# Kernel tuning notes

Hardware: AMD Instinct MI355X
Metric: run time of the kernel (lower is better)

Reference implementation:

```python
import jax, jax.numpy as jnp
import numpy as np

B, D, U = 8192, 1024, 1024


def setup_inputs() -> dict:
    key = jax.random.key(0)
    ks = jax.random.split(key, 11)
    scale = 0.05  # keras 'random_normal' initializer default stddev
    inp = {
        "inputs": jax.random.normal(ks[0], (B, D), jnp.float32),
        "h_tm1": jax.random.normal(ks[1], (B, U), jnp.float32),
        "c_tm1": jax.random.normal(ks[2], (B, U), jnp.float32),
        "W_i": jax.random.normal(ks[3], (D, U), jnp.float32) * scale,
        "U_i": jax.random.normal(ks[4], (U, U), jnp.float32) * scale,
        "b_i": jnp.zeros((U,), jnp.float32),
        "W_f": jax.random.normal(ks[5], (D, U), jnp.float32) * scale,
        "U_f": jax.random.normal(ks[6], (U, U), jnp.float32) * scale,
        "b_f": jnp.zeros((U,), jnp.float32),
        "W_c": jax.random.normal(ks[7], (D, U), jnp.float32) * scale,
        "U_c": jax.random.normal(ks[8], (U, U), jnp.float32) * scale,
        "b_c": jnp.zeros((U,), jnp.float32),
        "W_o": jax.random.normal(ks[9], (D, U), jnp.float32) * scale,
        "U_o": jax.random.normal(ks[10], (U, U), jnp.float32) * scale,
        "b_o": jnp.zeros((U,), jnp.float32),
    }
    return inp


def reference(inputs, h_tm1, c_tm1, W_i, U_i, b_i, W_f, U_f, b_f, W_c, U_c, b_c, W_o, U_o, b_o):
    # Concatenate the 4 gate projections into single GEMMs (same math, fused form)
    Wx = jnp.concatenate([W_i, W_f, W_c, W_o], axis=1)  # [D, 4U]
    Uh = jnp.concatenate([U_i, U_f, U_c, U_o], axis=1)  # [U, 4U]
    b = jnp.concatenate([b_i, b_f, b_c, b_o], axis=0)   # [4U]
    z = inputs @ Wx + h_tm1 @ Uh + b                     # [B, 4U]
    u = W_i.shape[1]
    zi, zf, zc, zo = z[:, :u], z[:, u:2 * u], z[:, 2 * u:3 * u], z[:, 3 * u:]
    i = jax.nn.sigmoid(zi)
    f = jax.nn.sigmoid(zf)
    c_ = jnp.tanh(zc)
    c = f * c_tm1 + i * c_
    o = jax.nn.sigmoid(zo)
    h = o * jnp.tanh(c)
    return (h, c)
```

## Files before the change

### kernel.cpp

```cpp
#include <hip/hip_runtime.h>
#include <hip/hip_bf16.h>
#include <cstdint>


using f32x4  = __attribute__((ext_vector_type(4))) float;
using short8 = __attribute__((ext_vector_type(8))) short;

__device__ __forceinline__ unsigned short f2bf(float f) {
  union { float f; unsigned int u; } v; v.f = f;
  unsigned int r = v.u + 0x7fffu + ((v.u >> 16) & 1u);
  return (unsigned short)(r >> 16);
}
__device__ __forceinline__ float sigmoidf_fast(float x) { return 1.f / (1.f + __expf(-x)); }
__device__ __forceinline__ float tanhf_fast(float x)    { return 1.f - 2.f / (__expf(2.f * x) + 1.f); }

__global__ void conv_a_kernel(const float* __restrict__ X, const float* __restrict__ H,
                              unsigned short* __restrict__ Abf) {
  int idx = blockIdx.x * blockDim.x + threadIdx.x;
  int b  = idx >> 8;
  int kq = (idx & 255) << 2;
  float4 x = *(const float4*)(X + (long)b * 1024 + kq);
  float4 h = *(const float4*)(H + (long)b * 1024 + kq);
  ushort4 xo, ho;
  xo.x = f2bf(x.x); xo.y = f2bf(x.y); xo.z = f2bf(x.z); xo.w = f2bf(x.w);
  ho.x = f2bf(h.x); ho.y = f2bf(h.y); ho.z = f2bf(h.z); ho.w = f2bf(h.w);
  *(ushort4*)(Abf + (long)b * 2048 + kq)        = xo;
  *(ushort4*)(Abf + (long)b * 2048 + 1024 + kq) = ho;
}

__global__ void conv_b_kernel(const float* W_i, const float* U_i,
                              const float* W_f, const float* U_f,
                              const float* W_c, const float* U_c,
                              const float* W_o, const float* U_o,
                              unsigned short* __restrict__ Bt) {
  __shared__ float tile[64][65];
  int z = blockIdx.z;
  const float* src;
  switch (z) {
    case 0: src = W_i; break; case 1: src = U_i; break;
    case 2: src = W_f; break; case 3: src = U_f; break;
    case 4: src = W_c; break; case 5: src = U_c; break;
    case 6: src = W_o; break; default: src = U_o; break;
  }
  int g = z >> 1, s = z & 1;
  int k0 = blockIdx.x * 64;
  int u0 = blockIdx.y * 64;
  int t = threadIdx.x;
  int c = t & 63, r0 = t >> 6;
#pragma unroll
  for (int i = 0; i < 16; ++i) {
    int r = i * 4 + r0;
    tile[r][c] = src[(long)(k0 + r) * 1024 + u0 + c];
  }
  __syncthreads();
  int ul = t >> 2;
  int ks = (t & 3) * 16;
  unsigned short outv[16];
#pragma unroll
  for (int j = 0; j < 16; ++j) outv[j] = f2bf(tile[ks + j][ul]);
  long n   = 4L * u0 + (ul >> 4) * 64 + g * 16 + (ul & 15);
  long col = (long)s * 1024 + k0 + ks;
  uint4* dst = (uint4*)(Bt + n * 2048 + col);
  dst[0] = *(uint4*)(outv);
  dst[1] = *(uint4*)(outv + 8);
}

__global__ __launch_bounds__(512) void lstm_gemm_kernel(
    const unsigned short* __restrict__ Abf,
    const unsigned short* __restrict__ Btbf,
    const float* __restrict__ b_i, const float* __restrict__ b_f,
    const float* __restrict__ b_c, const float* __restrict__ b_o,
    const float* __restrict__ c_tm1,
    float* __restrict__ outH, float* __restrict__ outC) {
  __shared__ unsigned short smem[3 * 16384];

  int bid = blockIdx.x;
  int swz = (bid & 7) * 64 + (bid >> 3);
  int bm = swz >> 4;
  int bn = swz & 15;

  int t = threadIdx.x;
  int lane = t & 63;
  int w = t >> 6;
  int wm = w >> 2;
  int wn = w & 3;
  int rl = lane & 15;
  int kg = lane >> 4;

#define AOFF(MI) ((wm * 128 + (MI) * 16 + rl) * 32 + \
    ((((kg * 16) ^ ((((wm * 128 + (MI) * 16 + rl) >> 1) & 3) << 4))) >> 1))
#define BOFF(NI) ((wn * 64 + (NI) * 16 + rl) * 32 + \
    ((((kg * 16) ^ ((((wn * 64 + (NI) * 16 + rl) >> 1) & 3) << 4))) >> 1))
  const int offA0 = AOFF(0), offA1 = AOFF(1), offA2 = AOFF(2), offA3 = AOFF(3);
  const int offA4 = AOFF(4), offA5 = AOFF(5), offA6 = AOFF(6), offA7 = AOFF(7);
  const int offB0 = 8192 + BOFF(0), offB1 = 8192 + BOFF(1);
  const int offB2 = 8192 + BOFF(2), offB3 = 8192 + BOFF(3);
#undef AOFF
#undef BOFF

  int srow = t >> 2;
  int cbe  = (((t & 3) * 16) ^ (((srow >> 1) & 3) << 4)) >> 1;
  const unsigned short* aS0 = Abf  + (long)(bm * 256 + srow) * 2048 + cbe;
  const unsigned short* aS1 = aS0 + 128L * 2048;
  const unsigned short* bS0 = Btbf + (long)(bn * 256 + srow) * 2048 + cbe;
  const unsigned short* bS1 = bS0 + 128L * 2048;
  const int dstA0 = t * 8, dstA1 = 4096 + t * 8;
  const int dstB0 = 8192 + t * 8, dstB1 = 12288 + t * 8;

#define GLL(SRC, SB, DOFF)                                                                     \
  __builtin_amdgcn_global_load_lds((const __attribute__((address_space(1))) void*)(SRC),       \
      (__attribute__((address_space(3))) void*)(&smem[(SB) * 16384 + (DOFF)]), 16, 0, 0)

  f32x4 acc[8][4];
#pragma unroll
  for (int mi = 0; mi < 8; ++mi)
#pragma unroll
    for (int ni = 0; ni < 4; ++ni) acc[mi][ni] = (f32x4){0.f, 0.f, 0.f, 0.f};

  GLL(aS0, 0, dstA0); GLL(aS1, 0, dstA1); GLL(bS0, 0, dstB0); GLL(bS1, 0, dstB1);
  GLL(aS0 + 32, 1, dstA0); GLL(aS1 + 32, 1, dstA1);
  GLL(bS0 + 32, 1, dstB0); GLL(bS1 + 32, 1, dstB1);
  asm volatile("s_waitcnt vmcnt(4)" ::: "memory");
  __builtin_amdgcn_s_barrier();
  aS0 += 64; aS1 += 64; bS0 += 64; bS1 += 64;

#define MF_ROW(AF, MI)                                                                  \
  acc[MI][0] = __builtin_amdgcn_mfma_f32_16x16x32_bf16(AF, bfr0, acc[MI][0], 0, 0, 0);  \
  acc[MI][1] = __builtin_amdgcn_mfma_f32_16x16x32_bf16(AF, bfr1, acc[MI][1], 0, 0, 0);  \
  acc[MI][2] = __builtin_amdgcn_mfma_f32_16x16x32_bf16(AF, bfr2, acc[MI][2], 0, 0, 0);  \
  acc[MI][3] = __builtin_amdgcn_mfma_f32_16x16x32_bf16(AF, bfr3, acc[MI][3], 0, 0, 0);

#define ITER(RBUF, SBUF, KOFF, DOSTAGE, VMN)                                   \
  do {                                                                         \
    const unsigned short* As_ = smem + (RBUF) * 16384;                         \
                      \
    short8 bfr0 = *(const short8*)(As_ + offB0);                               \
    short8 bfr1 = *(const short8*)(As_ + offB1);                               \
    short8 bfr2 = *(const short8*)(As_ + offB2);                               \
    short8 bfr3 = *(const short8*)(As_ + offB3);                               \
    short8 a0_ = *(const short8*)(As_ + offA0);                                \
    short8 a1_ = *(const short8*)(As_ + offA1);                                \
    short8 a2_ = *(const short8*)(As_ + offA2);                                \
    short8 a3_ = *(const short8*)(As_ + offA3);                                \
    if (DOSTAGE) { GLL(aS0 + (KOFF), (SBUF), dstA0); GLL(aS1 + (KOFF), (SBUF), dstA1); } \
    __builtin_amdgcn_s_barrier();                                              \
    asm volatile("s_waitcnt lgkmcnt(0)" ::: "memory");                         \
    __builtin_amdgcn_sched_barrier(0);                                         \
    __builtin_amdgcn_s_setprio(1);                                             \
    MF_ROW(a0_, 0) MF_ROW(a1_, 1) MF_ROW(a2_, 2) MF_ROW(a3_, 3)                \
    __builtin_amdgcn_s_setprio(0);                                             \
    __builtin_amdgcn_sched_barrier(0);                                         \
    __builtin_amdgcn_s_barrier();                                              \
                 \
    short8 a4_ = *(const short8*)(As_ + offA4);                                \
    short8 a5_ = *(const short8*)(As_ + offA5);                                \
    short8 a6_ = *(const short8*)(As_ + offA6);                                \
    short8 a7_ = *(const short8*)(As_ + offA7);                                \
    if (DOSTAGE) { GLL(bS0 + (KOFF), (SBUF), dstB0); GLL(bS1 + (KOFF), (SBUF), dstB1); } \
    if ((VMN) == 4) asm volatile("s_waitcnt vmcnt(4)" ::: "memory");           \
    if ((VMN) == 0) asm volatile("s_waitcnt vmcnt(0)" ::: "memory");           \
    __builtin_amdgcn_s_barrier();                                              \
    asm volatile("s_waitcnt lgkmcnt(0)" ::: "memory");                         \
    __builtin_amdgcn_sched_barrier(0);                                         \
    __builtin_amdgcn_s_setprio(1);                                             \
    MF_ROW(a4_, 4) MF_ROW(a5_, 5) MF_ROW(a6_, 6) MF_ROW(a7_, 7)                \
    __builtin_amdgcn_s_setprio(0);                                             \
    __builtin_amdgcn_sched_barrier(0);                                         \
    __builtin_amdgcn_s_barrier();                                              \
  } while (0)

  for (int g = 0; g < 20; ++g) {
    ITER(0, 2, 0,  1, 4);
    ITER(1, 0, 32, 1, 4);
    ITER(2, 1, 64, 1, 4);
    aS0 += 96; aS1 += 96; bS0 += 96; bS1 += 96;
  }
  ITER(0, 2, 0,  1, 4);
  ITER(1, 0, 32, 1, 4);
  ITER(2, 0, 0,  0, 0);
  ITER(0, 0, 0,  0, -1);
#undef ITER
#undef MF_ROW
#undef GLL

  int mbase = bm * 256 + wm * 128;
  int nbase = bn * 256 + wn * 64;
  int u = (nbase >> 2) + rl;
  float bi_v = b_i[u], bf_v = b_f[u], bc_v = b_c[u], bo_v = b_o[u];
  int rquad = (lane >> 4) << 2;
#pragma unroll
  for (int mi = 0; mi < 8; ++mi) {
#pragma unroll
    for (int j = 0; j < 4; ++j) {
      int brow = mbase + mi * 16 + rquad + j;
      float zi = acc[mi][0][j] + bi_v;
      float zf = acc[mi][1][j] + bf_v;
      float zc = acc[mi][2][j] + bc_v;
      float zo = acc[mi][3][j] + bo_v;
      float ig = sigmoidf_fast(zi);
      float fg = sigmoidf_fast(zf);
      float cg = tanhf_fast(zc);
      float og = sigmoidf_fast(zo);
      float cp = c_tm1[(long)brow * 1024 + u];
      float cn = fg * cp + ig * cg;
      float hn = og * tanhf_fast(cn);
      outH[(long)brow * 1024 + u] = hn;
      outC[(long)brow * 1024 + u] = cn;
    }
  }
}

extern "C" void kernel_launch(void* const* d_in, const int* in_sizes, int n_in,
                              void* d_out, int out_size, void* d_ws, size_t ws_size,
                              hipStream_t stream) {
  (void)in_sizes; (void)n_in; (void)out_size; (void)ws_size;
  const float* X   = (const float*)d_in[0];
  const float* Hst = (const float*)d_in[1];
  const float* Cst = (const float*)d_in[2];
  const float* W_i = (const float*)d_in[3];
  const float* U_i = (const float*)d_in[4];
  const float* b_i = (const float*)d_in[5];
  const float* W_f = (const float*)d_in[6];
  const float* U_f = (const float*)d_in[7];
  const float* b_f = (const float*)d_in[8];
  const float* W_c = (const float*)d_in[9];
  const float* U_c = (const float*)d_in[10];
  const float* b_c = (const float*)d_in[11];
  const float* W_o = (const float*)d_in[12];
  const float* U_o = (const float*)d_in[13];
  const float* b_o = (const float*)d_in[14];

  unsigned short* Abf  = (unsigned short*)d_ws;
  unsigned short* Btbf = (unsigned short*)((char*)d_ws + 33554432);

  float* outH = (float*)d_out;
  float* outC = outH + 8192L * 1024;

  conv_a_kernel<<<8192, 256, 0, stream>>>(X, Hst, Abf);
  conv_b_kernel<<<dim3(16, 16, 8), 256, 0, stream>>>(W_i, U_i, W_f, U_f, W_c, U_c, W_o, U_o, Btbf);
  lstm_gemm_kernel<<<512, 512, 0, stream>>>(Abf, Btbf, b_i, b_f, b_c, b_o, Cst, outH, outC);
}
```

Measured before the change: 164.4 us.

## Register-prefetch next LDS fragments and halve barriers in LSTM GEMM main loop

Restructures the GEMM k-loop so the A/B fragments for the next stage are loaded from LDS into a second register set (ping-pong p/q) while the current stage's MFMAs run. It cuts the barriers per k-step from four to one, issues all four global-to-LDS loads together after a vmcnt(0) wait, and unrolls the loop by six stages. It also sets launch_bounds(512,2), which caps registers to allow two blocks per CU. The extra fragment registers under a tighter register cap risk spills. The vmcnt(0) wait each step may also expose global load latency.

```diff
diff --git a/kernel.cpp b/kernel.cpp
--- a/kernel.cpp
+++ b/kernel.cpp
@@ -65,7 +65,7 @@
   dst[1] = *(uint4*)(outv + 8);
 }
 
-__global__ __launch_bounds__(512) void lstm_gemm_kernel(
+__global__ __launch_bounds__(512, 2) void lstm_gemm_kernel(
     const unsigned short* __restrict__ Abf,
     const unsigned short* __restrict__ Btbf,
     const float* __restrict__ b_i, const float* __restrict__ b_f,
@@ -117,70 +117,86 @@
 #pragma unroll
     for (int ni = 0; ni < 4; ++ni) acc[mi][ni] = (f32x4){0.f, 0.f, 0.f, 0.f};
 
+  short8 pa0, pa1, pa2, pa3, pb0, pb1, pb2, pb3;
+  short8 qa0, qa1, qa2, qa3, qb0, qb1, qb2, qb3;
+  short8 ah0, ah1, ah2, ah3;
+
   GLL(aS0, 0, dstA0); GLL(aS1, 0, dstA1); GLL(bS0, 0, dstB0); GLL(bS1, 0, dstB1);
   GLL(aS0 + 32, 1, dstA0); GLL(aS1 + 32, 1, dstA1);
   GLL(bS0 + 32, 1, dstB0); GLL(bS1 + 32, 1, dstB1);
   asm volatile("s_waitcnt vmcnt(4)" ::: "memory");
   __builtin_amdgcn_s_barrier();
+  pa0 = *(const short8*)(smem + offA0);
+  pa1 = *(const short8*)(smem + offA1);
+  pa2 = *(const short8*)(smem + offA2);
+  pa3 = *(const short8*)(smem + offA3);
+  pb0 = *(const short8*)(smem + offB0);
+  pb1 = *(const short8*)(smem + offB1);
+  pb2 = *(const short8*)(smem + offB2);
+  pb3 = *(const short8*)(smem + offB3);
   aS0 += 64; aS1 += 64; bS0 += 64; bS1 += 64;
 
-#define MF_ROW(AF, MI)                                                                  \
-  acc[MI][0] = __builtin_amdgcn_mfma_f32_16x16x32_bf16(AF, bfr0, acc[MI][0], 0, 0, 0);  \
-  acc[MI][1] = __builtin_amdgcn_mfma_f32_16x16x32_bf16(AF, bfr1, acc[MI][1], 0, 0, 0);  \
-  acc[MI][2] = __builtin_amdgcn_mfma_f32_16x16x32_bf16(AF, bfr2, acc[MI][2], 0, 0, 0);  \
-  acc[MI][3] = __builtin_amdgcn_mfma_f32_16x16x32_bf16(AF, bfr3, acc[MI][3], 0, 0, 0);
-
-#define ITER(RBUF, SBUF, KOFF, DOSTAGE, VMN)                                   \
+#define MF4(AF, MI, BP)                                                                      \
+  acc[MI][0] = __builtin_amdgcn_mfma_f32_16x16x32_bf16(AF, BP##0, acc[MI][0], 0, 0, 0);      \
+  acc[MI][1] = __builtin_amdgcn_mfma_f32_16x16x32_bf16(AF, BP##1, acc[MI][1], 0, 0, 0);      \
+  acc[MI][2] = __builtin_amdgcn_mfma_f32_16x16x32_bf16(AF, BP##2, acc[MI][2], 0, 0, 0);      \
+  acc[MI][3] = __builtin_amdgcn_mfma_f32_16x16x32_bf16(AF, BP##3, acc[MI][3], 0, 0, 0);
+
+#define ITER(BUF, STG, NXT, KOFF, C, N, DOSTAGE, DOPREF, DOSYNC)               \
   do {                                                                         \
-    const unsigned short* As_ = smem + (RBUF) * 16384;                         \
-                      \
-    short8 bfr0 = *(const short8*)(As_ + offB0);                               \
-    short8 bfr1 = *(const short8*)(As_ + offB1);                               \
-    short8 bfr2 = *(const short8*)(As_ + offB2);                               \
-    short8 bfr3 = *(const short8*)(As_ + offB3);                               \
-    short8 a0_ = *(const short8*)(As_ + offA0);                                \
-    short8 a1_ = *(const short8*)(As_ + offA1);                                \
-    short8 a2_ = *(const short8*)(As_ + offA2);                                \
-    short8 a3_ = *(const short8*)(As_ + offA3);                                \
-    if (DOSTAGE) { GLL(aS0 + (KOFF), (SBUF), dstA0); GLL(aS1 + (KOFF), (SBUF), dstA1); } \
-    __builtin_amdgcn_s_barrier();                                              \
-    asm volatile("s_waitcnt lgkmcnt(0)" ::: "memory");                         \
+    const unsigned short* Sr_ = smem + (BUF) * 16384;                          \
+    ah0 = *(const short8*)(Sr_ + offA4);                                       \
+    ah1 = *(const short8*)(Sr_ + offA5);                                       \
+    ah2 = *(const short8*)(Sr_ + offA6);                                       \
+    ah3 = *(const short8*)(Sr_ + offA7);                                       \
     __builtin_amdgcn_sched_barrier(0);                                         \
     __builtin_amdgcn_s_setprio(1);                                             \
-    MF_ROW(a0_, 0) MF_ROW(a1_, 1) MF_ROW(a2_, 2) MF_ROW(a3_, 3)                \
+    MF4(C##a0, 0, C##b) MF4(C##a1, 1, C##b)                                    \
+    MF4(C##a2, 2, C##b) MF4(C##a3, 3, C##b)                                    \
     __builtin_amdgcn_s_setprio(0);                                             \
     __builtin_amdgcn_sched_barrier(0);                                         \
-    __builtin_amdgcn_s_barrier();                                              \
-                 \
-    short8 a4_ = *(const short8*)(As_ + offA4);                                \
-    short8 a5_ = *(const short8*)(As_ + offA5);                                \
-    short8 a6_ = *(const short8*)(As_ + offA6);                                \
-    short8 a7_ = *(const short8*)(As_ + offA7);                                \
-    if (DOSTAGE) { GLL(bS0 + (KOFF), (SBUF), dstB0); GLL(bS1 + (KOFF), (SBUF), dstB1); } \
-    if ((VMN) == 4) asm volatile("s_waitcnt vmcnt(4)" ::: "memory");           \
-    if ((VMN) == 0) asm volatile("s_waitcnt vmcnt(0)" ::: "memory");           \
-    __builtin_amdgcn_s_barrier();                                              \
-    asm volatile("s_waitcnt lgkmcnt(0)" ::: "memory");                         \
+    if (DOSYNC) {                                                              \
+      asm volatile("s_waitcnt vmcnt(0)" ::: "memory");                         \
+      __builtin_amdgcn_s_barrier();                                            \
+      __builtin_amdgcn_sched_barrier(0);                                       \
+    }                                                                          \
+    if (DOSTAGE) {                                                             \
+      GLL(aS0 + (KOFF), (STG), dstA0); GLL(aS1 + (KOFF), (STG), dstA1);        \
+      GLL(bS0 + (KOFF), (STG), dstB0); GLL(bS1 + (KOFF), (STG), dstB1);        \
+    }                                                                          \
+    if (DOPREF) {                                                              \
+      const unsigned short* Sn_ = smem + (NXT) * 16384;                        \
+      N##a0 = *(const short8*)(Sn_ + offA0);                                   \
+      N##a1 = *(const short8*)(Sn_ + offA1);                                   \
+      N##a2 = *(const short8*)(Sn_ + offA2);                                   \
+      N##a3 = *(const short8*)(Sn_ + offA3);                                   \
+      N##b0 = *(const short8*)(Sn_ + offB0);                                   \
+      N##b1 = *(const short8*)(Sn_ + offB1);                                   \
+      N##b2 = *(const short8*)(Sn_ + offB2);                                   \
+      N##b3 = *(const short8*)(Sn_ + offB3);                                   \
+    }                                                                          \
     __builtin_amdgcn_sched_barrier(0);                                         \
     __builtin_amdgcn_s_setprio(1);                                             \
-    MF_ROW(a4_, 4) MF_ROW(a5_, 5) MF_ROW(a6_, 6) MF_ROW(a7_, 7)                \
+    MF4(ah0, 4, C##b) MF4(ah1, 5, C##b)                                        \
+    MF4(ah2, 6, C##b) MF4(ah3, 7, C##b)                                        \
     __builtin_amdgcn_s_setprio(0);                                             \
-    __builtin_amdgcn_sched_barrier(0);                                         \
-    __builtin_amdgcn_s_barrier();                                              \
   } while (0)
 
-  for (int g = 0; g < 20; ++g) {
-    ITER(0, 2, 0,  1, 4);
-    ITER(1, 0, 32, 1, 4);
-    ITER(2, 1, 64, 1, 4);
-    aS0 += 96; aS1 += 96; bS0 += 96; bS1 += 96;
-  }
-  ITER(0, 2, 0,  1, 4);
-  ITER(1, 0, 32, 1, 4);
-  ITER(2, 0, 0,  0, 0);
-  ITER(0, 0, 0,  0, -1);
+  for (int g = 0; g < 10; ++g) {
+    ITER(0, 2, 1, 0,   p, q, 1, 1, 1);
+    ITER(1, 0, 2, 32,  q, p, 1, 1, 1);
+    ITER(2, 1, 0, 64,  p, q, 1, 1, 1);
+    ITER(0, 2, 1, 96,  q, p, 1, 1, 1);
+    ITER(1, 0, 2, 128, p, q, 1, 1, 1);
+    ITER(2, 1, 0, 160, q, p, 1, 1, 1);
+    aS0 += 192; aS1 += 192; bS0 += 192; bS1 += 192;
+  }
+  ITER(0, 2, 1, 0,  p, q, 1, 1, 1);
+  ITER(1, 0, 2, 32, q, p, 1, 1, 1);
+  ITER(2, 0, 0, 0,  p, q, 0, 1, 1);
+  ITER(0, 0, 0, 0,  q, p, 0, 0, 0);
 #undef ITER
-#undef MF_ROW
+#undef MF4
 #undef GLL
 
   int mbase = bm * 256 + wm * 128;
```

Result: no change. 164.7 us (+0.2%).

## Restructure GEMM pipeline to 4-stage K-half LDS buffering with two blocks per CU

Applied to the files above, without the earlier changes.

Replaces the 3-buffer rotating LDS pipeline with a 4-deep pipeline split into separate A and B regions, each stage holding a 32-wide K slice, and rewrites the main loop as explicit phases that issue global-to-LDS loads further ahead. Adds a launch bound of 2 blocks per CU to limit register use. The goal is deeper prefetch to hide global load latency. The trade-off is that LDS grows to 128KB per block, which may prevent two blocks from actually co-residing, and the tighter register cap could cause spills.

```diff
diff --git a/kernel.cpp b/kernel.cpp
--- a/kernel.cpp
+++ b/kernel.cpp
@@ -65,14 +65,14 @@
   dst[1] = *(uint4*)(outv + 8);
 }
 
-__global__ __launch_bounds__(512) void lstm_gemm_kernel(
+__global__ __launch_bounds__(512, 2) void lstm_gemm_kernel(
     const unsigned short* __restrict__ Abf,
     const unsigned short* __restrict__ Btbf,
     const float* __restrict__ b_i, const float* __restrict__ b_f,
     const float* __restrict__ b_c, const float* __restrict__ b_o,
     const float* __restrict__ c_tm1,
     float* __restrict__ outH, float* __restrict__ outC) {
-  __shared__ unsigned short smem[3 * 16384];
+  __shared__ unsigned short smem[65536];
 
   int bid = blockIdx.x;
   int swz = (bid & 7) * 64 + (bid >> 3);
@@ -87,29 +87,39 @@
   int rl = lane & 15;
   int kg = lane >> 4;
 
-#define AOFF(MI) ((wm * 128 + (MI) * 16 + rl) * 32 + \
-    ((((kg * 16) ^ ((((wm * 128 + (MI) * 16 + rl) >> 1) & 3) << 4))) >> 1))
-#define BOFF(NI) ((wn * 64 + (NI) * 16 + rl) * 32 + \
-    ((((kg * 16) ^ ((((wn * 64 + (NI) * 16 + rl) >> 1) & 3) << 4))) >> 1))
-  const int offA0 = AOFF(0), offA1 = AOFF(1), offA2 = AOFF(2), offA3 = AOFF(3);
-  const int offA4 = AOFF(4), offA5 = AOFF(5), offA6 = AOFF(6), offA7 = AOFF(7);
-  const int offB0 = 8192 + BOFF(0), offB1 = 8192 + BOFF(1);
-  const int offB2 = 8192 + BOFF(2), offB3 = 8192 + BOFF(3);
-#undef AOFF
-#undef BOFF
+#define AOFFE(MI) ((wm * 128 + (MI) * 16 + rl) * 32 + \
+    ((kg ^ (((wm * 128 + (MI) * 16 + rl) >> 1) & 3)) << 3))
+#define BOFFE(NI) ((wn * 64 + (NI) * 16 + rl) * 32 + \
+    ((kg ^ (((wn * 64 + (NI) * 16 + rl) >> 1) & 3)) << 3))
+  const int offA0 = AOFFE(0), offA1 = AOFFE(1), offA2 = AOFFE(2), offA3 = AOFFE(3);
+  const int offA4 = AOFFE(4), offA5 = AOFFE(5), offA6 = AOFFE(6), offA7 = AOFFE(7);
+  const int offB0 = BOFFE(0), offB1 = BOFFE(1), offB2 = BOFFE(2), offB3 = BOFFE(3);
+#undef AOFFE
+#undef BOFFE
 
   int srow = t >> 2;
-  int cbe  = (((t & 3) * 16) ^ (((srow >> 1) & 3) << 4)) >> 1;
-  const unsigned short* aS0 = Abf  + (long)(bm * 256 + srow) * 2048 + cbe;
+  int ks   = (t & 3) ^ ((srow >> 1) & 3);
+  const unsigned short* aS0 = Abf  + (long)(bm * 256 + srow) * 2048 + ks * 8;
   const unsigned short* aS1 = aS0 + 128L * 2048;
-  const unsigned short* bS0 = Btbf + (long)(bn * 256 + srow) * 2048 + cbe;
+  const unsigned short* bS0 = Btbf + (long)(bn * 256 + srow) * 2048 + ks * 8;
   const unsigned short* bS1 = bS0 + 128L * 2048;
-  const int dstA0 = t * 8, dstA1 = 4096 + t * 8;
-  const int dstB0 = 8192 + t * 8, dstB1 = 12288 + t * 8;
-
-#define GLL(SRC, SB, DOFF)                                                                     \
-  __builtin_amdgcn_global_load_lds((const __attribute__((address_space(1))) void*)(SRC),       \
-      (__attribute__((address_space(3))) void*)(&smem[(SB) * 16384 + (DOFF)]), 16, 0, 0)
+  const int dA = t * 8;
+
+#define GLL(SRC, DELM)                                                                     \
+  __builtin_amdgcn_global_load_lds((const __attribute__((address_space(1))) void*)(SRC),   \
+      (__attribute__((address_space(3))) void*)(&smem[DELM]), 16, 0, 0)
+
+#define STAGE_A(SD, SKH, KOFF)                                                 \
+  do {                                                                         \
+    GLL(aS0 + (KOFF), (SD) * 16384 + (SKH) * 8192 + dA);                       \
+    GLL(aS1 + (KOFF), (SD) * 16384 + (SKH) * 8192 + 4096 + dA);                \
+  } while (0)
+#define STAGE_B(SD, SKH, KOFF)                                                 \
+  do {                                                                         \
+    GLL(bS0 + (KOFF), 32768 + (SD) * 16384 + (SKH) * 8192 + dA);               \
+    GLL(bS1 + (KOFF), 32768 + (SD) * 16384 + (SKH) * 8192 + 4096 + dA);        \
+  } while (0)
+#define VMC(N) asm volatile("s_waitcnt vmcnt(" #N ")" ::: "memory")
 
   f32x4 acc[8][4];
 #pragma unroll
@@ -117,70 +127,99 @@
 #pragma unroll
     for (int ni = 0; ni < 4; ++ni) acc[mi][ni] = (f32x4){0.f, 0.f, 0.f, 0.f};
 
-  GLL(aS0, 0, dstA0); GLL(aS1, 0, dstA1); GLL(bS0, 0, dstB0); GLL(bS1, 0, dstB1);
-  GLL(aS0 + 32, 1, dstA0); GLL(aS1 + 32, 1, dstA1);
-  GLL(bS0 + 32, 1, dstB0); GLL(bS1 + 32, 1, dstB1);
-  asm volatile("s_waitcnt vmcnt(4)" ::: "memory");
-  __builtin_amdgcn_s_barrier();
-  aS0 += 64; aS1 += 64; bS0 += 64; bS1 += 64;
-
-#define MF_ROW(AF, MI)                                                                  \
-  acc[MI][0] = __builtin_amdgcn_mfma_f32_16x16x32_bf16(AF, bfr0, acc[MI][0], 0, 0, 0);  \
-  acc[MI][1] = __builtin_amdgcn_mfma_f32_16x16x32_bf16(AF, bfr1, acc[MI][1], 0, 0, 0);  \
-  acc[MI][2] = __builtin_amdgcn_mfma_f32_16x16x32_bf16(AF, bfr2, acc[MI][2], 0, 0, 0);  \
-  acc[MI][3] = __builtin_amdgcn_mfma_f32_16x16x32_bf16(AF, bfr3, acc[MI][3], 0, 0, 0);
-
-#define ITER(RBUF, SBUF, KOFF, DOSTAGE, VMN)                                   \
-  do {                                                                         \
-    const unsigned short* As_ = smem + (RBUF) * 16384;                         \
-                      \
-    short8 bfr0 = *(const short8*)(As_ + offB0);                               \
-    short8 bfr1 = *(const short8*)(As_ + offB1);                               \
-    short8 bfr2 = *(const short8*)(As_ + offB2);                               \
-    short8 bfr3 = *(const short8*)(As_ + offB3);                               \
-    short8 a0_ = *(const short8*)(As_ + offA0);                                \
-    short8 a1_ = *(const short8*)(As_ + offA1);                                \
-    short8 a2_ = *(const short8*)(As_ + offA2);                                \
-    short8 a3_ = *(const short8*)(As_ + offA3);                                \
-    if (DOSTAGE) { GLL(aS0 + (KOFF), (SBUF), dstA0); GLL(aS1 + (KOFF), (SBUF), dstA1); } \
+  short8 aw0, aw1, aw2, aw3, bb0, bb1, bb2, bb3;
+
+#define MF4(AF, MI)                                                                      \
+  acc[MI][0] = __builtin_amdgcn_mfma_f32_16x16x32_bf16(AF, bb0, acc[MI][0], 0, 0, 0);    \
+  acc[MI][1] = __builtin_amdgcn_mfma_f32_16x16x32_bf16(AF, bb1, acc[MI][1], 0, 0, 0);    \
+  acc[MI][2] = __builtin_amdgcn_mfma_f32_16x16x32_bf16(AF, bb2, acc[MI][2], 0, 0, 0);    \
+  acc[MI][3] = __builtin_amdgcn_mfma_f32_16x16x32_bf16(AF, bb3, acc[MI][3], 0, 0, 0);
+
+#define PH_MH0(D, KK, STG, VM)                                                 \
+  {                                                                            \
+    const unsigned short* Ab_ = smem + (D) * 16384 + (KK) * 8192;              \
+    const unsigned short* Bb_ = smem + 32768 + (D) * 16384 + (KK) * 8192;      \
+    aw0 = *(const short8*)(Ab_ + offA0);                                       \
+    aw1 = *(const short8*)(Ab_ + offA1);                                       \
+    aw2 = *(const short8*)(Ab_ + offA2);                                       \
+    aw3 = *(const short8*)(Ab_ + offA3);                                       \
+    bb0 = *(const short8*)(Bb_ + offB0);                                       \
+    bb1 = *(const short8*)(Bb_ + offB1);                                       \
+    bb2 = *(const short8*)(Bb_ + offB2);                                       \
+    bb3 = *(const short8*)(Bb_ + offB3);                                       \
+    STG;                                                                       \
     __builtin_amdgcn_s_barrier();                                              \
     asm volatile("s_waitcnt lgkmcnt(0)" ::: "memory");                         \
     __builtin_amdgcn_sched_barrier(0);                                         \
     __builtin_amdgcn_s_setprio(1);                                             \
-    MF_ROW(a0_, 0) MF_ROW(a1_, 1) MF_ROW(a2_, 2) MF_ROW(a3_, 3)                \
+    MF4(aw0, 0) MF4(aw1, 1) MF4(aw2, 2) MF4(aw3, 3)                            \
     __builtin_amdgcn_s_setprio(0);                                             \
-    __builtin_amdgcn_sched_barrier(0);                                         \
-    __builtin_amdgcn_s_barrier();                                              \
-                 \
-    short8 a4_ = *(const short8*)(As_ + offA4);                                \
-    short8 a5_ = *(const short8*)(As_ + offA5);                                \
-    short8 a6_ = *(const short8*)(As_ + offA6);                                \
-    short8 a7_ = *(const short8*)(As_ + offA7);                                \
-    if (DOSTAGE) { GLL(bS0 + (KOFF), (SBUF), dstB0); GLL(bS1 + (KOFF), (SBUF), dstB1); } \
-    if ((VMN) == 4) asm volatile("s_waitcnt vmcnt(4)" ::: "memory");           \
-    if ((VMN) == 0) asm volatile("s_waitcnt vmcnt(0)" ::: "memory");           \
+    VM;                                                                        \
+    __builtin_amdgcn_s_barrier();                                              \
+  }
+
+#define PH_MH1(D, KK, STG, VM)                                                 \
+  {                                                                            \
+    const unsigned short* Ab_ = smem + (D) * 16384 + (KK) * 8192;              \
+    aw0 = *(const short8*)(Ab_ + offA4);                                       \
+    aw1 = *(const short8*)(Ab_ + offA5);                                       \
+    aw2 = *(const short8*)(Ab_ + offA6);                                       \
+    aw3 = *(const short8*)(Ab_ + offA7);                                       \
+    STG;                                                                       \
     __builtin_amdgcn_s_barrier();                                              \
     asm volatile("s_waitcnt lgkmcnt(0)" ::: "memory");                         \
     __builtin_amdgcn_sched_barrier(0);                                         \
     __builtin_amdgcn_s_setprio(1);                                             \
-    MF_ROW(a4_, 4) MF_ROW(a5_, 5) MF_ROW(a6_, 6) MF_ROW(a7_, 7)                \
+    MF4(aw0, 4) MF4(aw1, 5) MF4(aw2, 6) MF4(aw3, 7)                            \
     __builtin_amdgcn_s_setprio(0);                                             \
-    __builtin_amdgcn_sched_barrier(0);                                         \
-    __builtin_amdgcn_s_barrier();                                              \
-  } while (0)
-
-  for (int g = 0; g < 20; ++g) {
-    ITER(0, 2, 0,  1, 4);
-    ITER(1, 0, 32, 1, 4);
-    ITER(2, 1, 64, 1, 4);
-    aS0 += 96; aS1 += 96; bS0 += 96; bS1 += 96;
-  }
-  ITER(0, 2, 0,  1, 4);
-  ITER(1, 0, 32, 1, 4);
-  ITER(2, 0, 0,  0, 0);
-  ITER(0, 0, 0,  0, -1);
-#undef ITER
-#undef MF_ROW
+    VM;                                                                        \
+    __builtin_amdgcn_s_barrier();                                              \
+  }
+
+  STAGE_A(0, 0, 0);  STAGE_B(0, 0, 0);
+  STAGE_A(0, 1, 32); STAGE_B(0, 1, 32);
+  STAGE_A(1, 0, 64); STAGE_B(1, 0, 64);
+  STAGE_A(1, 1, 96); STAGE_B(1, 1, 96);
+  VMC(8);
+  __builtin_amdgcn_s_barrier();
+
+  PH_MH0(0, 0, (void)0,             (void)0);
+  PH_MH1(0, 0, (void)0,             VMC(8));
+  PH_MH0(0, 1, STAGE_A(0, 0, 128),  (void)0);
+  PH_MH1(0, 1, STAGE_B(0, 0, 128),  VMC(8));
+  PH_MH0(1, 0, STAGE_A(0, 1, 160),  (void)0);
+  PH_MH1(1, 0, STAGE_B(0, 1, 160),  VMC(8));
+  PH_MH0(1, 1, STAGE_A(1, 0, 192),  (void)0);
+  PH_MH1(1, 1, STAGE_B(1, 0, 192),  VMC(8));
+  aS0 += 128; aS1 += 128; bS0 += 128; bS1 += 128;
+
+  for (int i = 1; i <= 14; ++i) {
+    PH_MH0(0, 0, STAGE_A(1, 1, 96),   (void)0);
+    PH_MH1(0, 0, STAGE_B(1, 1, 96),   VMC(8));
+    PH_MH0(0, 1, STAGE_A(0, 0, 128),  (void)0);
+    PH_MH1(0, 1, STAGE_B(0, 0, 128),  VMC(8));
+    PH_MH0(1, 0, STAGE_A(0, 1, 160),  (void)0);
+    PH_MH1(1, 0, STAGE_B(0, 1, 160),  VMC(8));
+    PH_MH0(1, 1, STAGE_A(1, 0, 192),  (void)0);
+    PH_MH1(1, 1, STAGE_B(1, 0, 192),  VMC(8));
+    aS0 += 128; aS1 += 128; bS0 += 128; bS1 += 128;
+  }
+
+  PH_MH0(0, 0, STAGE_A(1, 1, 96),   (void)0);
+  PH_MH1(0, 0, STAGE_B(1, 1, 96),   VMC(8));
+  PH_MH0(0, 1, (void)0,             (void)0);
+  PH_MH1(0, 1, (void)0,             VMC(4));
+  PH_MH0(1, 0, (void)0,             (void)0);
+  PH_MH1(1, 0, (void)0,             VMC(0));
+  PH_MH0(1, 1, (void)0,             (void)0);
+  PH_MH1(1, 1, (void)0,             (void)0);
+
+#undef PH_MH0
+#undef PH_MH1
+#undef MF4
+#undef VMC
+#undef STAGE_A
+#undef STAGE_B
 #undef GLL
 
   int mbase = bm * 256 + wm * 128;
```

Result: no change. 162.1 us (-1.4%).
